# Optimization experiments

Hardware: AMD Instinct MI355X
Metric: run time of the kernel (lower is better)

The kernel has to match this reference:

```python
import jax, jax.numpy as jnp
import numpy as np

D_MODEL = 1024
NHEAD = 16
HEAD_DIM = D_MODEL // NHEAD
B, T = 2, 2048


def setup_inputs() -> dict:
    key = jax.random.key(0)
    ks = jax.random.split(key, 12)
    s = 1.0 / np.sqrt(D_MODEL)
    return {
        "query": jax.random.normal(ks[0], (B, T, D_MODEL), jnp.float32),
        "key": jax.random.normal(ks[1], (B, T, D_MODEL), jnp.float32),
        "value": jax.random.normal(ks[2], (B, T, D_MODEL), jnp.float32),
        "key_padding_mask": jnp.zeros((B, T), dtype=bool),
        "attn_mask": jnp.zeros((T, T), jnp.float32),
        "stoich_frac": jax.random.uniform(ks[3], (B, T), jnp.float32),
        "Wq": jax.random.uniform(ks[4], (D_MODEL, D_MODEL), jnp.float32, -s, s),
        "bq": jnp.zeros((D_MODEL,), jnp.float32),
        "Wk": jax.random.uniform(ks[5], (D_MODEL, D_MODEL), jnp.float32, -s, s),
        "bk": jnp.zeros((D_MODEL,), jnp.float32),
        "Wv": jax.random.uniform(ks[6], (D_MODEL, D_MODEL), jnp.float32, -s, s),
        "bv": jnp.zeros((D_MODEL,), jnp.float32),
        "Wo": jax.random.uniform(ks[7], (D_MODEL, D_MODEL), jnp.float32, -s, s),
        "bo": jnp.zeros((D_MODEL,), jnp.float32),
        "stoich_alpha": jnp.float32(0.1),
    }


def reference(query, key, value, key_padding_mask, attn_mask, stoich_frac,
              Wq, bq, Wk, bk, Wv, bv, Wo, bo, stoich_alpha):
    Bq, Tq, _ = query.shape
    Tk = key.shape[1]
    scale = HEAD_DIM ** -0.5
    # Linear projections (torch Linear: x @ W.T + b), reshape to [B, H, T, Dh]
    Q = (query @ Wq.T + bq).reshape(Bq, Tq, NHEAD, HEAD_DIM).transpose(0, 2, 1, 3)
    K = (key @ Wk.T + bk).reshape(Bq, Tk, NHEAD, HEAD_DIM).transpose(0, 2, 1, 3)
    V = (value @ Wv.T + bv).reshape(Bq, Tk, NHEAD, HEAD_DIM).transpose(0, 2, 1, 3)
    # Scores [B, H, Tq, Tk]
    scores = jnp.einsum("bhqd,bhkd->bhqk", Q, K) * scale
    # Stoichiometric pairwise bias (T_q == T_k path)
    diff = stoich_frac[:, :, None] - stoich_frac[:, None, :]  # [B, Tq, Tk]
    bias = stoich_alpha * (jnp.log1p(jnp.abs(diff)) * jnp.sign(diff))
    scores = scores + bias[:, None, :, :]
    scores = scores + attn_mask  # broadcasts [Tq, Tk]
    scores = jnp.where(key_padding_mask[:, None, None, :], -jnp.inf, scores)
    probs = jax.nn.softmax(scores, axis=-1)
    # dropout: eval mode / p=0 -> identity
    out = jnp.einsum("bhqk,bhkd->bhqd", probs, V)
    out = out.transpose(0, 2, 1, 3).reshape(Bq, Tq, D_MODEL)
    return out @ Wo.T + bo
```

## Files before the change

kernel.cpp:

```cpp
#include <hip/hip_runtime.h>
#include <math.h>

typedef __bf16 bf16_t;
typedef __bf16 bf16x8 __attribute__((ext_vector_type(8)));
typedef __bf16 bf16x4 __attribute__((ext_vector_type(4)));
typedef float  f32x4  __attribute__((ext_vector_type(4)));

#define NHEAD 16
#define HDIM 64
#define DMODEL 1024
#define TSEQ 2048

#define SBAR() __builtin_amdgcn_s_barrier()
#define LGKM0() do { asm volatile("s_waitcnt lgkmcnt(0)" ::: "memory"); \
                     __builtin_amdgcn_sched_barrier(0); } while (0)

__device__ __forceinline__ f32x4 mfma16(bf16x8 a, bf16x8 b, f32x4 c) {
  return __builtin_amdgcn_mfma_f32_16x16x32_bf16(a, b, c, 0, 0, 0);
}

__device__ __forceinline__ void gload16(const bf16_t* g, bf16_t* l) {
  __builtin_amdgcn_global_load_lds((const __attribute__((address_space(1))) void*)g,
                                   (__attribute__((address_space(3))) void*)l, 16, 0, 0);
}

__device__ __forceinline__ unsigned pk2(float lo, float hi) {
  unsigned short a = __builtin_bit_cast(unsigned short, (__bf16)lo);
  unsigned short c = __builtin_bit_cast(unsigned short, (__bf16)hi);
  return ((unsigned)c << 16) | a;
}

__device__ __forceinline__ void cvtstore(f32x4 x0, f32x4 x1, bf16_t* dh, bf16_t* dl, int off) {
  bf16x8 hfr, lfr;
#pragma unroll
  for (int j = 0; j < 4; ++j) {
    float v = x0[j];
    __bf16 hb = (__bf16)v;
    hfr[j] = hb; lfr[j] = (__bf16)(v - (float)hb);
    float w = x1[j];
    __bf16 wb = (__bf16)w;
    hfr[4 + j] = wb; lfr[4 + j] = (__bf16)(w - (float)wb);
  }
  *(bf16x8*)(dh + off) = hfr;
  *(bf16x8*)(dl + off) = lfr;
}

__global__ __launch_bounds__(256)
void build_bias(const float* __restrict__ amask, const unsigned char* __restrict__ kpm,
                const float* __restrict__ sf, const float* __restrict__ alpha_p,
                bf16_t* __restrict__ BM) {
  size_t idx = (size_t)blockIdx.x * 256 + threadIdx.x;
  int k8 = (int)(idx & (TSEQ / 8 - 1));
  size_t bq = idx >> 8;
  int b = (int)(bq >> 11);
  int q = (int)(bq & (TSEQ - 1));
  const float sfq = sf[bq];
  const float alpha = *alpha_p;
  const float* sfk = sf + (size_t)b * TSEQ + k8 * 8;
  const float* am  = amask + (size_t)q * TSEQ + k8 * 8;
  const unsigned char* kp = kpm + (size_t)b * TSEQ + k8 * 8;
  bf16x8 o;
#pragma unroll
  for (int j = 0; j < 8; ++j) {
    float df = sfq - sfk[j];
    float v = alpha * copysignf(log1pf(fabsf(df)), df) + am[j];
    if (kp[j]) v = -1.0e30f;
    o[j] = (__bf16)v;
  }
  *(bf16x8*)&BM[idx * 8] = o;
}

template<int MODE>
__global__ __launch_bounds__(256)
void gemm_mfma(const float* __restrict__ A, const float* __restrict__ W,
               const float* __restrict__ bias,
               bf16_t* __restrict__ obh, bf16_t* __restrict__ obl,
               float* __restrict__ of) {
  __shared__ bf16_t AH[8 * 512], AL[8 * 512], WH[4 * 512], WL[4 * 512];
  const int tid = threadIdx.x;
  const int lane = tid & 63;
  const int a15 = lane & 15, g = lane >> 4;
  const int wv = tid >> 6, wm = wv >> 1, wn = wv & 1;
  const int m0 = blockIdx.y * 128, n0 = blockIdx.x * 64;
  constexpr int NI = (MODE == 2) ? 2 : 4;
  constexpr int NJ = (MODE == 2) ? 4 : 2;
  f32x4 acc[NI][NJ] = {};

  const int s0 = tid, s1 = tid + 256;
  const int t0 = s0 >> 6, l0 = s0 & 63;
  const int t1 = s1 >> 6, l1 = s1 & 63;
  const float* pA0 = A + (size_t)(m0 + t0 * 16 + (l0 & 15)) * DMODEL + 8 * (l0 >> 4);
  const float* pA1 = A + (size_t)(m0 + t1 * 16 + (l1 & 15)) * DMODEL + 8 * (l1 >> 4);
  const float* pW  = W + (size_t)(n0 + t0 * 16 + (l0 & 15)) * DMODEL + 8 * (l0 >> 4);

  f32x4 rA0a = *(const f32x4*)pA0, rA0b = *(const f32x4*)(pA0 + 4);
  f32x4 rA1a = *(const f32x4*)pA1, rA1b = *(const f32x4*)(pA1 + 4);
  f32x4 rWa  = *(const f32x4*)pW,  rWb  = *(const f32x4*)(pW + 4);

  for (int k0 = 0; k0 < DMODEL; k0 += 32) {
    SBAR();
    cvtstore(rA0a, rA0b, AH, AL, s0 * 8);
    cvtstore(rA1a, rA1b, AH, AL, s1 * 8);
    cvtstore(rWa,  rWb,  WH, WL, s0 * 8);
    __builtin_amdgcn_sched_barrier(0);
    if (k0 + 32 < DMODEL) {
      pA0 += 32; pA1 += 32; pW += 32;
      rA0a = *(const f32x4*)pA0; rA0b = *(const f32x4*)(pA0 + 4);
      rA1a = *(const f32x4*)pA1; rA1b = *(const f32x4*)(pA1 + 4);
      rWa  = *(const f32x4*)pW;  rWb  = *(const f32x4*)(pW + 4);
    }
    LGKM0();
    SBAR();

    bf16x8 ah[4], al[4], wh[2], wl[2];
#pragma unroll
    for (int i = 0; i < 4; ++i) {
      ah[i] = *(const bf16x8*)&AH[(wm * 4 + i) * 512 + lane * 8];
      al[i] = *(const bf16x8*)&AL[(wm * 4 + i) * 512 + lane * 8];
    }
#pragma unroll
    for (int j = 0; j < 2; ++j) {
      wh[j] = *(const bf16x8*)&WH[(wn * 2 + j) * 512 + lane * 8];
      wl[j] = *(const bf16x8*)&WL[(wn * 2 + j) * 512 + lane * 8];
    }
    __builtin_amdgcn_s_setprio(1);
    if (MODE == 2) {
#pragma unroll
      for (int i = 0; i < 2; ++i)
#pragma unroll
        for (int j = 0; j < 4; ++j) {
          acc[i][j] = mfma16(wh[i], ah[j], acc[i][j]);
          acc[i][j] = mfma16(wh[i], al[j], acc[i][j]);
          acc[i][j] = mfma16(wl[i], ah[j], acc[i][j]);
        }
    } else {
#pragma unroll
      for (int i = 0; i < 4; ++i)
#pragma unroll
        for (int j = 0; j < 2; ++j) {
          acc[i][j] = mfma16(ah[i], wh[j], acc[i][j]);
          acc[i][j] = mfma16(ah[i], wl[j], acc[i][j]);
          acc[i][j] = mfma16(al[i], wh[j], acc[i][j]);
        }
    }
    __builtin_amdgcn_s_setprio(0);
  }

  if (MODE == 0) {
#pragma unroll
    for (int i = 0; i < 4; ++i)
#pragma unroll
      for (int j = 0; j < 2; ++j) {
        int n = n0 + wn * 32 + j * 16 + a15;
        float bs = bias[n];
#pragma unroll
        for (int r = 0; r < 4; ++r) {
          int m = m0 + wm * 64 + i * 16 + 4 * g + r;
          of[(size_t)m * DMODEL + n] = acc[i][j][r] + bs;
        }
      }
  } else if (MODE == 1) {
#pragma unroll
    for (int i = 0; i < 4; ++i)
#pragma unroll
      for (int j = 0; j < 2; ++j) {
        int n = n0 + wn * 32 + j * 16 + a15;
        float bs = bias[n];
        int hh = n >> 6, d = n & 63;
#pragma unroll
        for (int r = 0; r < 4; ++r) {
          int m = m0 + wm * 64 + i * 16 + 4 * g + r;
          int bb = m >> 11, t = m & (TSEQ - 1);
          float v = acc[i][j][r] + bs;
          size_t o = (((size_t)(bb * NHEAD + hh)) * TSEQ + t) * HDIM + d;
          __bf16 hb = (__bf16)v;
          obh[o] = hb;
          obl[o] = (__bf16)(v - (float)hb);
        }
      }
  } else {
#pragma unroll
    for (int i = 0; i < 2; ++i)
#pragma unroll
      for (int j = 0; j < 4; ++j) {
        int m = m0 + wm * 64 + j * 16 + a15;
        int bb = m >> 11, t = m & (TSEQ - 1);
#pragma unroll
        for (int r = 0; r < 4; ++r) {
          int n = n0 + wn * 32 + i * 16 + 4 * g + r;
          float v = acc[i][j][r] + bias[n];
          int hh = n >> 6, d = n & 63;
          size_t o = (((size_t)(bb * NHEAD + hh)) * HDIM + d) * TSEQ + t;
          __bf16 hb = (__bf16)v;
          obh[o] = hb;
          obl[o] = (__bf16)(v - (float)hb);
        }
      }
  }
}

__global__ __launch_bounds__(512)
void attn_mfma(const bf16_t* __restrict__ Qhi, const bf16_t* __restrict__ Qlo,
               const bf16_t* __restrict__ Khi, const bf16_t* __restrict__ Klo,
               const bf16_t* __restrict__ Vth, const bf16_t* __restrict__ Vtl,
               const bf16_t* __restrict__ BMt, float* __restrict__ O) {
  __shared__ bf16_t KH[2][8 * 512], KL[2][8 * 512], VH[2][8 * 512], VL[2][8 * 512];
  const int tid = threadIdx.x;
  const int lane = tid & 63, wv = tid >> 6;
  const int a15 = lane & 15, g = lane >> 4;
  const int b = blockIdx.z, h = blockIdx.y, q0 = blockIdx.x * 128;
  const int bh = b * NHEAD + h;
  const int qg = q0 + wv * 16 + a15;
  constexpr int NT = TSEQ / 64;

  const bf16_t* Qh_b = Qhi + ((size_t)bh * TSEQ + qg) * HDIM;
  const bf16_t* Ql_b = Qlo + ((size_t)bh * TSEQ + qg) * HDIM;
  const bf16_t* Kh_b = Khi + (size_t)bh * TSEQ * HDIM;
  const bf16_t* Kl_b = Klo + (size_t)bh * TSEQ * HDIM;
  const bf16_t* Vh_b = Vth + (size_t)bh * HDIM * TSEQ;
  const bf16_t* Vl_b = Vtl + (size_t)bh * HDIM * TSEQ;
  const bf16_t* bmrow = BMt + ((size_t)b * TSEQ + qg) * TSEQ;

  bf16x8 qh[2], ql[2];
  qh[0] = *(const bf16x8*)&Qh_b[8 * g];
  qh[1] = *(const bf16x8*)&Qh_b[32 + 8 * g];
  ql[0] = *(const bf16x8*)&Ql_b[8 * g];
  ql[1] = *(const bf16x8*)&Ql_b[32 + 8 * g];

  f32x4 aco[4] = {};
  float m_run = -3.0e38f, l_run = 0.f;
  bf16x4 bmv[4], bmn[4];

  const int ts = wv >> 1, ks = wv & 1;
  auto stage = [&](int k0, int buf) {
    size_t ko = (size_t)(k0 + 16 * ts + a15) * HDIM + 32 * ks + 8 * g;
    gload16(Kh_b + ko, &KH[buf][wv * 512]);
    gload16(Kl_b + ko, &KL[buf][wv * 512]);
    size_t vo = (size_t)(16 * ts + a15) * TSEQ + k0 + 32 * ks + 8 * g;
    gload16(Vh_b + vo, &VH[buf][wv * 512]);
    gload16(Vl_b + vo, &VL[buf][wv * 512]);
  };

#pragma unroll
  for (int mt = 0; mt < 4; ++mt) bmv[mt] = *(const bf16x4*)&bmrow[16 * mt + 4 * g];
  stage(0, 0);

  for (int t = 0; t < NT; ++t) {
    const int cur = t & 1;
    if (t + 1 < NT) {
      const int kn = (t + 1) * 64;
#pragma unroll
      for (int mt = 0; mt < 4; ++mt) bmn[mt] = *(const bf16x4*)&bmrow[kn + 16 * mt + 4 * g];
      stage(kn, cur ^ 1);
      asm volatile("s_waitcnt vmcnt(8)" ::: "memory");
    } else {
      asm volatile("s_waitcnt vmcnt(0)" ::: "memory");
    }
    __builtin_amdgcn_sched_barrier(0);
    SBAR();

    f32x4 s4[4];
    __builtin_amdgcn_s_setprio(1);
#pragma unroll
    for (int mt = 0; mt < 4; ++mt) {
      bf16x8 k0h = *(const bf16x8*)&KH[cur][(mt * 2 + 0) * 512 + lane * 8];
      bf16x8 k1h = *(const bf16x8*)&KH[cur][(mt * 2 + 1) * 512 + lane * 8];
      bf16x8 k0l = *(const bf16x8*)&KL[cur][(mt * 2 + 0) * 512 + lane * 8];
      bf16x8 k1l = *(const bf16x8*)&KL[cur][(mt * 2 + 1) * 512 + lane * 8];
      f32x4 sa = {};
      sa = mfma16(k0h, qh[0], sa);
      sa = mfma16(k1h, qh[1], sa);
      sa = mfma16(k0h, ql[0], sa);
      sa = mfma16(k1h, ql[1], sa);
      sa = mfma16(k0l, qh[0], sa);
      sa = mfma16(k1l, qh[1], sa);
      s4[mt] = sa;
    }
    __builtin_amdgcn_s_setprio(0);

#pragma unroll
    for (int mt = 0; mt < 4; ++mt)
#pragma unroll
      for (int r = 0; r < 4; ++r)
        s4[mt][r] = fmaf(s4[mt][r], 0.125f, (float)bmv[mt][r]);

    float tmax = -3.0e38f;
#pragma unroll
    for (int mt = 0; mt < 4; ++mt)
#pragma unroll
      for (int r = 0; r < 4; ++r) tmax = fmaxf(tmax, s4[mt][r]);
    tmax = fmaxf(tmax, __shfl_xor(tmax, 16));
    tmax = fmaxf(tmax, __shfl_xor(tmax, 32));
    if (!__all(tmax - m_run <= 8.0f)) {
      float mnew = fmaxf(m_run, tmax);
      float corr = __expf(m_run - mnew);
      l_run *= corr;
#pragma unroll
      for (int dt = 0; dt < 4; ++dt) aco[dt] *= corr;
      m_run = mnew;
    }
    float psum = 0.f;
    unsigned pk01[4], pk23[4];
#pragma unroll
    for (int mt = 0; mt < 4; ++mt) {
      float p0 = __expf(s4[mt][0] - m_run);
      float p1 = __expf(s4[mt][1] - m_run);
      float p2 = __expf(s4[mt][2] - m_run);
      float p3 = __expf(s4[mt][3] - m_run);
      psum += (p0 + p1) + (p2 + p3);
      pk01[mt] = pk2(p0, p1);
      pk23[mt] = pk2(p2, p3);
    }
    psum += __shfl_xor(psum, 16);
    psum += __shfl_xor(psum, 32);
    l_run += psum;

    bf16x8 pf[2];
#pragma unroll
    for (int kss = 0; kss < 2; ++kss) {
      int src0 = a15 + 16 * (2 * (g & 1));
      int src1 = src0 + 16;
      unsigned A0 = __shfl(pk01[2 * kss + 0], src0), A1 = __shfl(pk01[2 * kss + 1], src0);
      unsigned B0 = __shfl(pk23[2 * kss + 0], src0), B1 = __shfl(pk23[2 * kss + 1], src0);
      unsigned C0 = __shfl(pk01[2 * kss + 0], src1), C1 = __shfl(pk01[2 * kss + 1], src1);
      unsigned D0 = __shfl(pk23[2 * kss + 0], src1), D1 = __shfl(pk23[2 * kss + 1], src1);
      bool hi2 = (g >> 1) & 1;
      uint4 wds;
      wds.x = hi2 ? A1 : A0;
      wds.y = hi2 ? B1 : B0;
      wds.z = hi2 ? C1 : C0;
      wds.w = hi2 ? D1 : D0;
      pf[kss] = __builtin_bit_cast(bf16x8, wds);
    }

    __builtin_amdgcn_s_setprio(1);
#pragma unroll
    for (int dt = 0; dt < 4; ++dt) {
#pragma unroll
      for (int kss = 0; kss < 2; ++kss) {
        bf16x8 vh = *(const bf16x8*)&VH[cur][(dt * 2 + kss) * 512 + lane * 8];
        bf16x8 vl = *(const bf16x8*)&VL[cur][(dt * 2 + kss) * 512 + lane * 8];
        aco[dt] = mfma16(vh, pf[kss], aco[dt]);
        aco[dt] = mfma16(vl, pf[kss], aco[dt]);
      }
    }
    __builtin_amdgcn_s_setprio(0);

    if (t + 1 < NT) {
#pragma unroll
      for (int mt = 0; mt < 4; ++mt) bmv[mt] = bmn[mt];
    }
    SBAR();
  }

  float inv = 1.0f / l_run;
#pragma unroll
  for (int dt = 0; dt < 4; ++dt) {
    f32x4 o = aco[dt] * inv;
    *(f32x4*)&O[((size_t)b * TSEQ + qg) * DMODEL + h * HDIM + dt * 16 + 4 * g] = o;
  }
}

extern "C" void kernel_launch(void* const* d_in, const int* in_sizes, int n_in,
                              void* d_out, int out_size, void* d_ws, size_t ws_size,
                              hipStream_t stream) {
  const float* query = (const float*)d_in[0];
  const float* key = (const float*)d_in[1];
  const float* value = (const float*)d_in[2];
  const unsigned char* kpm = (const unsigned char*)d_in[3];
  const float* amask = (const float*)d_in[4];
  const float* sf = (const float*)d_in[5];
  const float* Wq = (const float*)d_in[6];
  const float* bq = (const float*)d_in[7];
  const float* Wk = (const float*)d_in[8];
  const float* bk = (const float*)d_in[9];
  const float* Wv = (const float*)d_in[10];
  const float* bv = (const float*)d_in[11];
  const float* Wo = (const float*)d_in[12];
  const float* bo = (const float*)d_in[13];
  const float* alpha = (const float*)d_in[14];
  float* out = (float*)d_out;

  const size_t NEL = (size_t)2 * NHEAD * TSEQ * HDIM;
  bf16_t* p = (bf16_t*)d_ws;
  bf16_t* Qh = p;
  bf16_t* Ql = p + NEL;
  bf16_t* Kh = p + 2 * NEL;
  bf16_t* Kl = p + 3 * NEL;
  bf16_t* Vh = p + 4 * NEL;
  bf16_t* Vl = p + 5 * NEL;
  float* Oa = (float*)(p + 6 * NEL);
  bf16_t* BMt = (bf16_t*)(Oa + (size_t)4096 * DMODEL);

  dim3 bb(256);
  build_bias<<<dim3(4096), bb, 0, stream>>>(amask, kpm, sf, alpha, BMt);

  dim3 gg(16, 32);
  gemm_mfma<1><<<gg, bb, 0, stream>>>(query, Wq, bq, Qh, Ql, nullptr);
  gemm_mfma<1><<<gg, bb, 0, stream>>>(key, Wk, bk, Kh, Kl, nullptr);
  gemm_mfma<2><<<gg, bb, 0, stream>>>(value, Wv, bv, Vh, Vl, nullptr);
  dim3 ga(TSEQ / 128, NHEAD, 2);
  attn_mfma<<<ga, dim3(512), 0, stream>>>(Qh, Ql, Kh, Kl, Vh, Vl, BMt, Oa);
  gemm_mfma<0><<<gg, bb, 0, stream>>>(Oa, Wo, bo, nullptr, nullptr, out);
}
```

Measured before the change: 339.9 us.

## Use 512-thread GEMM blocks and route attention P fragments through LDS

The projection GEMMs now launch 512 threads per block, so each of the 8 waves computes a 32x32 sub-tile instead of 64x32. The W tile is loaded by only the first 256 threads, which adds divergent branches. In attention, the cross-lane shuffle sequence that rearranges the softmax probabilities into MFMA B-operand layout is replaced by a swizzled write to a per-wave LDS scratch buffer followed by one vector read. This is meant to add latency hiding and cut shuffle instructions, at the cost of extra LDS traffic, an lgkmcnt wait, and lower MFMA work per wave in the GEMMs.

Measured after the change: 338.7 us. Within noise of the previous version (-0.4%).

```diff
diff --git a/kernel.cpp b/kernel.cpp
--- a/kernel.cpp
+++ b/kernel.cpp
@@ -71,7 +71,7 @@
 }
 
 template<int MODE>
-__global__ __launch_bounds__(256)
+__global__ __launch_bounds__(512)
 void gemm_mfma(const float* __restrict__ A, const float* __restrict__ W,
                const float* __restrict__ bias,
                bf16_t* __restrict__ obh, bf16_t* __restrict__ obl,
@@ -82,60 +82,53 @@
   const int a15 = lane & 15, g = lane >> 4;
   const int wv = tid >> 6, wm = wv >> 1, wn = wv & 1;
   const int m0 = blockIdx.y * 128, n0 = blockIdx.x * 64;
-  constexpr int NI = (MODE == 2) ? 2 : 4;
-  constexpr int NJ = (MODE == 2) ? 4 : 2;
-  f32x4 acc[NI][NJ] = {};
-
-  const int s0 = tid, s1 = tid + 256;
-  const int t0 = s0 >> 6, l0 = s0 & 63;
-  const int t1 = s1 >> 6, l1 = s1 & 63;
+  f32x4 acc[2][2] = {};
+
+  const int t0 = tid >> 6, l0 = tid & 63;
   const float* pA0 = A + (size_t)(m0 + t0 * 16 + (l0 & 15)) * DMODEL + 8 * (l0 >> 4);
-  const float* pA1 = A + (size_t)(m0 + t1 * 16 + (l1 & 15)) * DMODEL + 8 * (l1 >> 4);
-  const float* pW  = W + (size_t)(n0 + t0 * 16 + (l0 & 15)) * DMODEL + 8 * (l0 >> 4);
+  const bool doW = (tid < 256);
+  const int sW = tid & 255;
+  const int tw = sW >> 6, lw = sW & 63;
+  const float* pW = W + (size_t)(n0 + tw * 16 + (lw & 15)) * DMODEL + 8 * (lw >> 4);
 
   f32x4 rA0a = *(const f32x4*)pA0, rA0b = *(const f32x4*)(pA0 + 4);
-  f32x4 rA1a = *(const f32x4*)pA1, rA1b = *(const f32x4*)(pA1 + 4);
-  f32x4 rWa  = *(const f32x4*)pW,  rWb  = *(const f32x4*)(pW + 4);
+  f32x4 rWa = {}, rWb = {};
+  if (doW) { rWa = *(const f32x4*)pW; rWb = *(const f32x4*)(pW + 4); }
 
   for (int k0 = 0; k0 < DMODEL; k0 += 32) {
     SBAR();
-    cvtstore(rA0a, rA0b, AH, AL, s0 * 8);
-    cvtstore(rA1a, rA1b, AH, AL, s1 * 8);
-    cvtstore(rWa,  rWb,  WH, WL, s0 * 8);
+    cvtstore(rA0a, rA0b, AH, AL, tid * 8);
+    if (doW) cvtstore(rWa, rWb, WH, WL, sW * 8);
     __builtin_amdgcn_sched_barrier(0);
     if (k0 + 32 < DMODEL) {
-      pA0 += 32; pA1 += 32; pW += 32;
+      pA0 += 32;
       rA0a = *(const f32x4*)pA0; rA0b = *(const f32x4*)(pA0 + 4);
-      rA1a = *(const f32x4*)pA1; rA1b = *(const f32x4*)(pA1 + 4);
-      rWa  = *(const f32x4*)pW;  rWb  = *(const f32x4*)(pW + 4);
+      if (doW) { pW += 32; rWa = *(const f32x4*)pW; rWb = *(const f32x4*)(pW + 4); }
     }
     LGKM0();
     SBAR();
 
-    bf16x8 ah[4], al[4], wh[2], wl[2];
-#pragma unroll
-    for (int i = 0; i < 4; ++i) {
-      ah[i] = *(const bf16x8*)&AH[(wm * 4 + i) * 512 + lane * 8];
-      al[i] = *(const bf16x8*)&AL[(wm * 4 + i) * 512 + lane * 8];
-    }
-#pragma unroll
-    for (int j = 0; j < 2; ++j) {
-      wh[j] = *(const bf16x8*)&WH[(wn * 2 + j) * 512 + lane * 8];
-      wl[j] = *(const bf16x8*)&WL[(wn * 2 + j) * 512 + lane * 8];
+    bf16x8 ah[2], al[2], wh[2], wl[2];
+#pragma unroll
+    for (int i = 0; i < 2; ++i) {
+      ah[i] = *(const bf16x8*)&AH[(wm * 2 + i) * 512 + lane * 8];
+      al[i] = *(const bf16x8*)&AL[(wm * 2 + i) * 512 + lane * 8];
+      wh[i] = *(const bf16x8*)&WH[(wn * 2 + i) * 512 + lane * 8];
+      wl[i] = *(const bf16x8*)&WL[(wn * 2 + i) * 512 + lane * 8];
     }
     __builtin_amdgcn_s_setprio(1);
     if (MODE == 2) {
 #pragma unroll
       for (int i = 0; i < 2; ++i)
 #pragma unroll
-        for (int j = 0; j < 4; ++j) {
+        for (int j = 0; j < 2; ++j) {
           acc[i][j] = mfma16(wh[i], ah[j], acc[i][j]);
           acc[i][j] = mfma16(wh[i], al[j], acc[i][j]);
           acc[i][j] = mfma16(wl[i], ah[j], acc[i][j]);
         }
     } else {
 #pragma unroll
-      for (int i = 0; i < 4; ++i)
+      for (int i = 0; i < 2; ++i)
 #pragma unroll
         for (int j = 0; j < 2; ++j) {
           acc[i][j] = mfma16(ah[i], wh[j], acc[i][j]);
@@ -148,20 +141,20 @@
 
   if (MODE == 0) {
 #pragma unroll
-    for (int i = 0; i < 4; ++i)
+    for (int i = 0; i < 2; ++i)
 #pragma unroll
       for (int j = 0; j < 2; ++j) {
         int n = n0 + wn * 32 + j * 16 + a15;
         float bs = bias[n];
 #pragma unroll
         for (int r = 0; r < 4; ++r) {
-          int m = m0 + wm * 64 + i * 16 + 4 * g + r;
+          int m = m0 + wm * 32 + i * 16 + 4 * g + r;
           of[(size_t)m * DMODEL + n] = acc[i][j][r] + bs;
         }
       }
   } else if (MODE == 1) {
 #pragma unroll
-    for (int i = 0; i < 4; ++i)
+    for (int i = 0; i < 2; ++i)
 #pragma unroll
       for (int j = 0; j < 2; ++j) {
         int n = n0 + wn * 32 + j * 16 + a15;
@@ -169,7 +162,7 @@
         int hh = n >> 6, d = n & 63;
 #pragma unroll
         for (int r = 0; r < 4; ++r) {
-          int m = m0 + wm * 64 + i * 16 + 4 * g + r;
+          int m = m0 + wm * 32 + i * 16 + 4 * g + r;
           int bb = m >> 11, t = m & (TSEQ - 1);
           float v = acc[i][j][r] + bs;
           size_t o = (((size_t)(bb * NHEAD + hh)) * TSEQ + t) * HDIM + d;
@@ -182,8 +175,8 @@
 #pragma unroll
     for (int i = 0; i < 2; ++i)
 #pragma unroll
-      for (int j = 0; j < 4; ++j) {
-        int m = m0 + wm * 64 + j * 16 + a15;
+      for (int j = 0; j < 2; ++j) {
+        int m = m0 + wm * 32 + j * 16 + a15;
         int bb = m >> 11, t = m & (TSEQ - 1);
 #pragma unroll
         for (int r = 0; r < 4; ++r) {
@@ -205,6 +198,7 @@
                const bf16_t* __restrict__ Vth, const bf16_t* __restrict__ Vtl,
                const bf16_t* __restrict__ BMt, float* __restrict__ O) {
   __shared__ bf16_t KH[2][8 * 512], KL[2][8 * 512], VH[2][8 * 512], VL[2][8 * 512];
+  __shared__ bf16_t PS[8 * 512];
   const int tid = threadIdx.x;
   const int lane = tid & 63, wv = tid >> 6;
   const int a15 = lane & 15, g = lane >> 4;
@@ -315,33 +309,28 @@
     psum += __shfl_xor(psum, 32);
     l_run += psum;
 
-    bf16x8 pf[2];
+    const int psb = wv * 512 + a15 * 32;
+    const int r3 = a15 & 3;
+    __builtin_amdgcn_s_setprio(1);
 #pragma unroll
     for (int kss = 0; kss < 2; ++kss) {
-      int src0 = a15 + 16 * (2 * (g & 1));
-      int src1 = src0 + 16;
-      unsigned A0 = __shfl(pk01[2 * kss + 0], src0), A1 = __shfl(pk01[2 * kss + 1], src0);
-      unsigned B0 = __shfl(pk23[2 * kss + 0], src0), B1 = __shfl(pk23[2 * kss + 1], src0);
-      unsigned C0 = __shfl(pk01[2 * kss + 0], src1), C1 = __shfl(pk01[2 * kss + 1], src1);
-      unsigned D0 = __shfl(pk23[2 * kss + 0], src1), D1 = __shfl(pk23[2 * kss + 1], src1);
-      bool hi2 = (g >> 1) & 1;
-      uint4 wds;
-      wds.x = hi2 ? A1 : A0;
-      wds.y = hi2 ? B1 : B0;
-      wds.z = hi2 ? C1 : C0;
-      wds.w = hi2 ? D1 : D0;
-      pf[kss] = __builtin_bit_cast(bf16x8, wds);
-    }
-
-    __builtin_amdgcn_s_setprio(1);
-#pragma unroll
-    for (int dt = 0; dt < 4; ++dt) {
-#pragma unroll
-      for (int kss = 0; kss < 2; ++kss) {
+#pragma unroll
+      for (int mh = 0; mh < 2; ++mh) {
+        int mt = kss * 2 + mh;
+        int phys = ((mh << 1) | (g >> 1)) ^ r3;
+        uint2 w2;
+        w2.x = pk01[mt];
+        w2.y = pk23[mt];
+        *(uint2*)&PS[psb + phys * 8 + (g & 1) * 4] = w2;
+      }
+      LGKM0();
+      bf16x8 pf = *(const bf16x8*)&PS[psb + ((g ^ r3) << 3)];
+#pragma unroll
+      for (int dt = 0; dt < 4; ++dt) {
         bf16x8 vh = *(const bf16x8*)&VH[cur][(dt * 2 + kss) * 512 + lane * 8];
         bf16x8 vl = *(const bf16x8*)&VL[cur][(dt * 2 + kss) * 512 + lane * 8];
-        aco[dt] = mfma16(vh, pf[kss], aco[dt]);
-        aco[dt] = mfma16(vl, pf[kss], aco[dt]);
+        aco[dt] = mfma16(vh, pf, aco[dt]);
+        aco[dt] = mfma16(vl, pf, aco[dt]);
       }
     }
     __builtin_amdgcn_s_setprio(0);
@@ -392,14 +381,13 @@
   float* Oa = (float*)(p + 6 * NEL);
   bf16_t* BMt = (bf16_t*)(Oa + (size_t)4096 * DMODEL);
 
-  dim3 bb(256);
-  build_bias<<<dim3(4096), bb, 0, stream>>>(amask, kpm, sf, alpha, BMt);
-
-  dim3 gg(16, 32);
-  gemm_mfma<1><<<gg, bb, 0, stream>>>(query, Wq, bq, Qh, Ql, nullptr);
-  gemm_mfma<1><<<gg, bb, 0, stream>>>(key, Wk, bk, Kh, Kl, nullptr);
-  gemm_mfma<2><<<gg, bb, 0, stream>>>(value, Wv, bv, Vh, Vl, nullptr);
+  build_bias<<<dim3(4096), dim3(256), 0, stream>>>(amask, kpm, sf, alpha, BMt);
+
+  dim3 gg(16, 32), gb(512);
+  gemm_mfma<1><<<gg, gb, 0, stream>>>(query, Wq, bq, Qh, Ql, nullptr);
+  gemm_mfma<1><<<gg, gb, 0, stream>>>(key, Wk, bk, Kh, Kl, nullptr);
+  gemm_mfma<2><<<gg, gb, 0, stream>>>(value, Wv, bv, Vh, Vl, nullptr);
   dim3 ga(TSEQ / 128, NHEAD, 2);
   attn_mfma<<<ga, dim3(512), 0, stream>>>(Qh, Ql, Kh, Kl, Vh, Vl, BMt, Oa);
-  gemm_mfma<0><<<gg, bb, 0, stream>>>(Oa, Wo, bo, nullptr, nullptr, out);
-}
+  gemm_mfma<0><<<gg, gb, 0, stream>>>(Oa, Wo, bo, nullptr, nullptr, out);
+}
```
